# Performance work log

Measured on AMD Instinct MI355X. Metric: run time of the kernel, lower is better.

The kernel has to match this reference:

```python
import jax, jax.numpy as jnp
import numpy as np
from jax import lax

KH, KW = 3, 3  # hardcoded in the original extract_patches sizes=(1,3,3,1)


def setup_inputs() -> dict:
    key = jax.random.key(0)
    k1, k2, k3 = jax.random.split(key, 3)
    B, H, W, C = 32, 56, 56, 128
    num_och = 256
    x = jax.random.normal(k1, (B, H, W, C), dtype=jnp.float32)
    w = jax.random.normal(k2, (num_och, KH * KW * C), dtype=jnp.float32) * 0.05
    b = jax.random.normal(k3, (num_och,), dtype=jnp.float32) * 0.05
    return {"x": x, "w": w, "b": b}


def reference(x, w, b):
    # Original: extract_patches (SAME, stride 1, 3x3) -> tile num_och times ->
    # elementwise multiply with w -> reduce_sum over patch axis -> + bias.
    # This is exactly a 3x3 SAME conv: patch layout is (ky, kx, cin) row-major,
    # matching tf.image.extract_patches depth ordering.
    num_och = w.shape[0]
    cin = x.shape[-1]
    # (num_och, KH*KW*C) -> (KH, KW, C, num_och) for HWIO kernel layout
    kernel = w.reshape(num_och, KH, KW, cin).transpose(1, 2, 3, 0)
    out = lax.conv_general_dilated(
        x, kernel,
        window_strides=(1, 1),
        padding="SAME",
        dimension_numbers=("NHWC", "HWIO", "NHWC"),
    )
    return out + b
```

## Files before the change

kernel.cpp:

```cpp
#include <hip/hip_runtime.h>
#include <hip/hip_bf16.h>

#define HH   56
#define WW_  56
#define CIN  128
#define OCH  256
#define NPIX (32*56*56)
#define NX   (NPIX*CIN)
#define NW   (OCH*9*CIN)
#define XB_BYTES ((size_t)NX*2)
#define WB_BYTES ((size_t)NW*2)
#define ZP_OFF   (XB_BYTES + WB_BYTES)
#define WS_NEEDED (ZP_OFF + 256)

#define BM 128
#define BN 128
#define THREADS 256

typedef __attribute__((ext_vector_type(8))) short bf16x8;
typedef __attribute__((ext_vector_type(4))) float f32x4;
typedef __attribute__((address_space(1))) void v_g;
typedef __attribute__((address_space(3))) void v_l;

__device__ __forceinline__ unsigned short f2bf(float f) {
  union { float f; unsigned u; } v; v.f = f;
  unsigned r = v.u + 0x7FFF + ((v.u >> 16) & 1);
  return (unsigned short)(r >> 16);
}

__global__ __launch_bounds__(256) void convert_kern(
    const float* __restrict__ x, const float* __restrict__ w,
    char* __restrict__ ws)
{
  if (blockIdx.x == 0 && threadIdx.x < 64)
    ((float*)(ws + ZP_OFF))[threadIdx.x] = 0.f;

  unsigned short* out = (unsigned short*)ws;
  const int NT8 = (NX + NW) / 8;
  for (int i = blockIdx.x * blockDim.x + threadIdx.x; i < NT8;
       i += gridDim.x * blockDim.x) {
    const int e = i * 8;
    const float* src = (e < NX) ? (x + e) : (w + (e - NX));
    const float4 a = ((const float4*)src)[0];
    const float4 b = ((const float4*)src)[1];
    union { bf16x8 v; unsigned short u[8]; } p;
    p.u[0] = f2bf(a.x); p.u[1] = f2bf(a.y); p.u[2] = f2bf(a.z); p.u[3] = f2bf(a.w);
    p.u[4] = f2bf(b.x); p.u[5] = f2bf(b.y); p.u[6] = f2bf(b.z); p.u[7] = f2bf(b.w);
    *(bf16x8*)(out + e) = p.v;
  }
}

__global__ __launch_bounds__(THREADS, 2) void conv_gemm(
    const char* __restrict__ ws, const float* __restrict__ bias,
    float* __restrict__ out)
{
  __shared__ char lds[2][32768];

  const char* xb = ws;
  const char* wb = ws + XB_BYTES;
  const char* zp = ws + ZP_OFF;

  const int tid  = threadIdx.x;
  const int lane = tid & 63;
  const int wv   = tid >> 6;
  const int m0   = (blockIdx.x >> 1) * BM;
  const int n0   = (blockIdx.x & 1) * BN;

  int pixA[4]; int phA_[4]; int pwA_[4]; int chkA[4]; const char* bsrcB[4];
#pragma unroll
  for (int c = 0; c < 4; ++c) {
    const int rloc  = wv * 32 + c * 8 + (lane >> 3);
    const int chunk = ((lane & 7) ^ (rloc & 7)) * 16;
    chkA[c] = chunk;
    const int p   = m0 + rloc;
    const int pb  = p / (HH * WW_);
    const int phw = p - pb * (HH * WW_);
    phA_[c] = phw / WW_;
    pwA_[c] = phw - phA_[c] * WW_;
    pixA[c] = p;
    bsrcB[c] = wb + (size_t)(n0 + rloc) * (9 * CIN * 2) + chunk;
  }

  const int fr = lane & 15;
  const int fq = lane >> 4;
  const int wm = (wv >> 1) * 64;
  const int wn = (wv & 1) * 64;

  int aoff[2][4], boff[2][4];
#pragma unroll
  for (int ks = 0; ks < 2; ++ks)
#pragma unroll
    for (int i = 0; i < 4; ++i) {
      const int r = wm + i * 16 + fr;
      aoff[ks][i] = r * 128 + ((ks * 64 + fq * 16) ^ ((r & 7) << 4));
      const int c = wn + i * 16 + fr;
      boff[ks][i] = 16384 + c * 128 + ((ks * 64 + fq * 16) ^ ((c & 7) << 4));
    }

  f32x4 acc[4][4];
  const f32x4 zero4 = {0.f, 0.f, 0.f, 0.f};
#pragma unroll
  for (int i = 0; i < 4; ++i)
#pragma unroll
    for (int j = 0; j < 4; ++j) acc[i][j] = zero4;

#define STAGE(tt, bb) do {                                                   \
    const int kpos_ = (tt) >> 1, kc_ = (tt) & 1;                             \
    const int ky_ = kpos_ / 3;                                               \
    const int dy_ = ky_ - 1, dx_ = kpos_ - ky_ * 3 - 1;                      \
    _Pragma("unroll")                                                        \
    for (int c = 0; c < 4; ++c) {                                            \
      const int ih_ = phA_[c] + dy_, iw_ = pwA_[c] + dx_;                    \
      const bool v_ = ((unsigned)ih_ < (unsigned)HH) &                       \
                      ((unsigned)iw_ < (unsigned)WW_);                       \
      const char* ga_ = v_ ? (xb + (size_t)(pixA[c] + dy_ * WW_ + dx_) * 256 \
                                 + kc_ * 128 + chkA[c])                      \
                           : (zp + chkA[c]);                                 \
      __builtin_amdgcn_global_load_lds((const v_g*)ga_,                      \
          (v_l*)(&lds[bb][0] + wv * 4096 + c * 1024), 16, 0, 0);             \
      const char* gb_ = bsrcB[c] + (tt) * 128;                               \
      __builtin_amdgcn_global_load_lds((const v_g*)gb_,                      \
          (v_l*)(&lds[bb][16384] + wv * 4096 + c * 1024), 16, 0, 0);         \
    }                                                                        \
  } while (0)

  STAGE(0, 0);
  __syncthreads();

#pragma unroll 2
  for (int t = 0; t < 18; ++t) {
    if (t < 17) STAGE(t + 1, (t + 1) & 1);

    const char* base = &lds[t & 1][0];
    bf16x8 A[2][4], Bv[2][4];
#pragma unroll
    for (int ks = 0; ks < 2; ++ks)
#pragma unroll
      for (int i = 0; i < 4; ++i) {
        A[ks][i]  = *(const bf16x8*)(base + aoff[ks][i]);
        Bv[ks][i] = *(const bf16x8*)(base + boff[ks][i]);
      }
#pragma unroll
    for (int ks = 0; ks < 2; ++ks)
#pragma unroll
      for (int mi = 0; mi < 4; ++mi)
#pragma unroll
        for (int nj = 0; nj < 4; ++nj)
          acc[mi][nj] = __builtin_amdgcn_mfma_f32_16x16x32_bf16(
              A[ks][mi], Bv[ks][nj], acc[mi][nj], 0, 0, 0);

    __syncthreads();
  }
#undef STAGE

  float bv[4];
#pragma unroll
  for (int j = 0; j < 4; ++j) bv[j] = bias[n0 + wn + j * 16 + fr];

#pragma unroll
  for (int mi = 0; mi < 4; ++mi) {
#pragma unroll
    for (int j = 0; j < 4; ++j) {
      const int prow = m0 + wm + mi * 16 + fq * 4 + j;
      float* orow = out + (size_t)prow * OCH + n0 + wn + fr;
#pragma unroll
      for (int ni = 0; ni < 4; ++ni)
        orow[ni * 16] = acc[mi][ni][j] + bv[ni];
    }
  }
}

__global__ __launch_bounds__(THREADS) void conv3x3_mfma_fb(
    const float* __restrict__ x, const float* __restrict__ w,
    const float* __restrict__ bias, float* __restrict__ out)
{
  __shared__ alignas(16) unsigned char As[BM * 64];
  __shared__ alignas(16) unsigned char Bs[BN * 64];

  const int tid = threadIdx.x;
  const int m0 = (blockIdx.x >> 1) * BM;
  const int n0 = (blockIdx.x & 1) * BN;

  const int srow = tid >> 1;
  const int soff = (tid & 1) * 16;

  const int p   = m0 + srow;
  const int pb  = p / (HH * WW_);
  const int phw = p - pb * (HH * WW_);
  const int ph  = phw / WW_;
  const int pw  = phw - ph * WW_;

  const float* xrow = x + ((size_t)((pb * HH + ph) * WW_ + pw)) * CIN + soff;
  const float* wrow = w + (size_t)(n0 + srow) * (9 * CIN) + soff;

  const int sw0 = (srow * 64 + soff * 2)      ^ ((srow & 7) << 4);
  const int sw1 = (srow * 64 + soff * 2 + 16) ^ ((srow & 7) << 4);

  const int lane = tid & 63;
  const int wv = tid >> 6;
  const int wm = (wv >> 1) * 64;
  const int wn = (wv & 1) * 64;
  const int fr = lane & 15;
  const int fq = lane >> 4;

  int aoff[4], boff[4];
#pragma unroll
  for (int i = 0; i < 4; ++i) {
    const int r = wm + i * 16 + fr;
    aoff[i] = (r * 64 + fq * 16) ^ ((r & 7) << 4);
    const int c = wn + i * 16 + fr;
    boff[i] = (c * 64 + fq * 16) ^ ((c & 7) << 4);
  }

  f32x4 acc[4][4];
  const f32x4 zero4 = {0.f, 0.f, 0.f, 0.f};
#pragma unroll
  for (int i = 0; i < 4; ++i)
#pragma unroll
    for (int j = 0; j < 4; ++j) acc[i][j] = zero4;

#pragma unroll 1
  for (int kpos = 0; kpos < 9; ++kpos) {
    const int ky = kpos / 3;
    const int kx = kpos - ky * 3;
    const int ih = ph + ky - 1;
    const int iw = pw + kx - 1;
    const bool valid = ((unsigned)ih < (unsigned)HH) & ((unsigned)iw < (unsigned)WW_);
    const float* asrc = xrow + ((ky - 1) * WW_ + (kx - 1)) * CIN;
    const float* bsrc = wrow + kpos * CIN;

#pragma unroll 1
    for (int kc = 0; kc < 4; ++kc) {
      float4 a0, a1, a2, a3;
      if (valid) {
        const float4* s = (const float4*)(asrc + kc * 32);
        a0 = s[0]; a1 = s[1]; a2 = s[2]; a3 = s[3];
      } else {
        a0 = make_float4(0.f, 0.f, 0.f, 0.f);
        a1 = a0; a2 = a0; a3 = a0;
      }
      const float4* tql = (const float4*)(bsrc + kc * 32);
      const float4 b0 = tql[0], b1 = tql[1], b2 = tql[2], b3 = tql[3];

      __syncthreads();

      union { bf16x8 v; unsigned short u[8]; } pA0, pA1, pB0, pB1;
      pA0.u[0] = f2bf(a0.x); pA0.u[1] = f2bf(a0.y); pA0.u[2] = f2bf(a0.z); pA0.u[3] = f2bf(a0.w);
      pA0.u[4] = f2bf(a1.x); pA0.u[5] = f2bf(a1.y); pA0.u[6] = f2bf(a1.z); pA0.u[7] = f2bf(a1.w);
      pA1.u[0] = f2bf(a2.x); pA1.u[1] = f2bf(a2.y); pA1.u[2] = f2bf(a2.z); pA1.u[3] = f2bf(a2.w);
      pA1.u[4] = f2bf(a3.x); pA1.u[5] = f2bf(a3.y); pA1.u[6] = f2bf(a3.z); pA1.u[7] = f2bf(a3.w);
      pB0.u[0] = f2bf(b0.x); pB0.u[1] = f2bf(b0.y); pB0.u[2] = f2bf(b0.z); pB0.u[3] = f2bf(b0.w);
      pB0.u[4] = f2bf(b1.x); pB0.u[5] = f2bf(b1.y); pB0.u[6] = f2bf(b1.z); pB0.u[7] = f2bf(b1.w);
      pB1.u[0] = f2bf(b2.x); pB1.u[1] = f2bf(b2.y); pB1.u[2] = f2bf(b2.z); pB1.u[3] = f2bf(b2.w);
      pB1.u[4] = f2bf(b3.x); pB1.u[5] = f2bf(b3.y); pB1.u[6] = f2bf(b3.z); pB1.u[7] = f2bf(b3.w);

      *(bf16x8*)(As + sw0) = pA0.v;
      *(bf16x8*)(As + sw1) = pA1.v;
      *(bf16x8*)(Bs + sw0) = pB0.v;
      *(bf16x8*)(Bs + sw1) = pB1.v;

      __syncthreads();

      bf16x8 af[4], bfr[4];
#pragma unroll
      for (int i = 0; i < 4; ++i) af[i]  = *(const bf16x8*)(As + aoff[i]);
#pragma unroll
      for (int j = 0; j < 4; ++j) bfr[j] = *(const bf16x8*)(Bs + boff[j]);
#pragma unroll
      for (int i = 0; i < 4; ++i)
#pragma unroll
        for (int j = 0; j < 4; ++j)
          acc[i][j] = __builtin_amdgcn_mfma_f32_16x16x32_bf16(af[i], bfr[j], acc[i][j], 0, 0, 0);
    }
  }

  float bv[4];
#pragma unroll
  for (int j = 0; j < 4; ++j) bv[j] = bias[n0 + wn + j * 16 + fr];

#pragma unroll
  for (int mi = 0; mi < 4; ++mi) {
#pragma unroll
    for (int j = 0; j < 4; ++j) {
      const int prow = m0 + wm + mi * 16 + fq * 4 + j;
      float* orow = out + (size_t)prow * OCH + n0 + wn + fr;
#pragma unroll
      for (int ni = 0; ni < 4; ++ni)
        orow[ni * 16] = acc[mi][ni][j] + bv[ni];
    }
  }
}

extern "C" void kernel_launch(void* const* d_in, const int* in_sizes, int n_in,
                              void* d_out, int out_size, void* d_ws, size_t ws_size,
                              hipStream_t stream) {
  (void)in_sizes; (void)n_in; (void)out_size;
  const float* x = (const float*)d_in[0];
  const float* w = (const float*)d_in[1];
  const float* b = (const float*)d_in[2];
  float* out = (float*)d_out;

  if (ws_size >= WS_NEEDED) {
    convert_kern<<<dim3(2048), dim3(256), 0, stream>>>(x, w, (char*)d_ws);
    const int grid = (NPIX / BM) * (OCH / BN);
    conv_gemm<<<dim3(grid), dim3(THREADS), 0, stream>>>((const char*)d_ws, b, out);
  } else {
    const int grid = (NPIX / BM) * (OCH / BN);
    conv3x3_mfma_fb<<<dim3(grid), dim3(THREADS), 0, stream>>>(x, w, b, out);
  }
}
```

Baseline: 204.7 us.

## Triple-buffer conv GEMM with 512 threads and explicit waitcnt pipelining

Rewrites the implicit-GEMM conv kernel to use 8 waves per block (each computing a 64x32 sub-tile) and a three-slot LDS ring buffer. Loads are prefetched two stages ahead, and raw s_barrier plus partial vmcnt waits replace the full __syncthreads. MFMA sections run at raised wave priority. The aim is to hide global-to-LDS latency and raise occupancy per CU, at the cost of 96KB LDS per block and a fragile manual waitcnt schedule.

```diff
diff --git a/kernel.cpp b/kernel.cpp
--- a/kernel.cpp
+++ b/kernel.cpp
@@ -13,9 +13,9 @@
 #define ZP_OFF   (XB_BYTES + WB_BYTES)
 #define WS_NEEDED (ZP_OFF + 256)
 
-#define BM 128
-#define BN 128
-#define THREADS 256
+#define NT   18
+#define SLOT 32768
+#define THREADS 512
 
 typedef __attribute__((ext_vector_type(8))) short bf16x8;
 typedef __attribute__((ext_vector_type(4))) float f32x4;
@@ -50,11 +50,11 @@
   }
 }
 
-__global__ __launch_bounds__(THREADS, 2) void conv_gemm(
+__global__ __launch_bounds__(THREADS, 2) void conv_gemm3(
     const char* __restrict__ ws, const float* __restrict__ bias,
     float* __restrict__ out)
 {
-  __shared__ char lds[2][32768];
+  __shared__ char lds[3 * SLOT];
 
   const char* xb = ws;
   const char* wb = ws + XB_BYTES;
@@ -62,124 +62,158 @@
 
   const int tid  = threadIdx.x;
   const int lane = tid & 63;
-  const int wv   = tid >> 6;
-  const int m0   = (blockIdx.x >> 1) * BM;
-  const int n0   = (blockIdx.x & 1) * BN;
-
-  int pixA[4]; int phA_[4]; int pwA_[4]; int chkA[4]; const char* bsrcB[4];
-#pragma unroll
-  for (int c = 0; c < 4; ++c) {
-    const int rloc  = wv * 32 + c * 8 + (lane >> 3);
-    const int chunk = ((lane & 7) ^ (rloc & 7)) * 16;
-    chkA[c] = chunk;
-    const int p   = m0 + rloc;
-    const int pb  = p / (HH * WW_);
-    const int phw = p - pb * (HH * WW_);
-    phA_[c] = phw / WW_;
-    pwA_[c] = phw - phA_[c] * WW_;
-    pixA[c] = p;
-    bsrcB[c] = wb + (size_t)(n0 + rloc) * (9 * CIN * 2) + chunk;
+  const int m0   = (blockIdx.x >> 1) * 128;
+  const int n0   = (blockIdx.x & 1) * 128;
+
+  const int r0  = tid >> 3;
+  const int chk = ((tid & 7) ^ (r0 & 7)) * 16;
+  const char* zpc = zp + chk;
+
+  int pixA[2], phA[2], pwA[2];
+  const char* bsrc[2];
+#pragma unroll
+  for (int l = 0; l < 2; ++l) {
+    const int r  = r0 + l * 64;
+    const int p  = m0 + r;
+    const int pb = p / 3136;
+    const int phw = p - pb * 3136;
+    phA[l] = phw / 56;
+    pwA[l] = phw - phA[l] * 56;
+    pixA[l] = p;
+    bsrc[l] = wb + (size_t)(n0 + r) * 2304 + chk;
   }
 
   const int fr = lane & 15;
   const int fq = lane >> 4;
-  const int wm = (wv >> 1) * 64;
-  const int wn = (wv & 1) * 64;
-
-  int aoff[2][4], boff[2][4];
-#pragma unroll
-  for (int ks = 0; ks < 2; ++ks)
-#pragma unroll
-    for (int i = 0; i < 4; ++i) {
-      const int r = wm + i * 16 + fr;
-      aoff[ks][i] = r * 128 + ((ks * 64 + fq * 16) ^ ((r & 7) << 4));
-      const int c = wn + i * 16 + fr;
-      boff[ks][i] = 16384 + c * 128 + ((ks * 64 + fq * 16) ^ ((c & 7) << 4));
-    }
-
-  f32x4 acc[4][4];
+  const int wv = tid >> 6;
+  const int wr = wv >> 2;
+  const int wc = wv & 3;
+
+  int aoff[2][4], boff[2][2];
+#pragma unroll
+  for (int ks = 0; ks < 2; ++ks) {
+#pragma unroll
+    for (int mi = 0; mi < 4; ++mi) {
+      const int r = wr * 64 + mi * 16 + fr;
+      aoff[ks][mi] = r * 128 + ((ks * 64 + fq * 16) ^ ((r & 7) << 4));
+    }
+#pragma unroll
+    for (int nj = 0; nj < 2; ++nj) {
+      const int c = wc * 32 + nj * 16 + fr;
+      boff[ks][nj] = 16384 + c * 128 + ((ks * 64 + fq * 16) ^ ((c & 7) << 4));
+    }
+  }
+
+  f32x4 acc[4][2];
   const f32x4 zero4 = {0.f, 0.f, 0.f, 0.f};
 #pragma unroll
-  for (int i = 0; i < 4; ++i)
-#pragma unroll
-    for (int j = 0; j < 4; ++j) acc[i][j] = zero4;
-
-#define STAGE(tt, bb) do {                                                   \
-    const int kpos_ = (tt) >> 1, kc_ = (tt) & 1;                             \
-    const int ky_ = kpos_ / 3;                                               \
-    const int dy_ = ky_ - 1, dx_ = kpos_ - ky_ * 3 - 1;                      \
-    _Pragma("unroll")                                                        \
-    for (int c = 0; c < 4; ++c) {                                            \
-      const int ih_ = phA_[c] + dy_, iw_ = pwA_[c] + dx_;                    \
-      const bool v_ = ((unsigned)ih_ < (unsigned)HH) &                       \
-                      ((unsigned)iw_ < (unsigned)WW_);                       \
-      const char* ga_ = v_ ? (xb + (size_t)(pixA[c] + dy_ * WW_ + dx_) * 256 \
-                                 + kc_ * 128 + chkA[c])                      \
-                           : (zp + chkA[c]);                                 \
-      __builtin_amdgcn_global_load_lds((const v_g*)ga_,                      \
-          (v_l*)(&lds[bb][0] + wv * 4096 + c * 1024), 16, 0, 0);             \
-      const char* gb_ = bsrcB[c] + (tt) * 128;                               \
-      __builtin_amdgcn_global_load_lds((const v_g*)gb_,                      \
-          (v_l*)(&lds[bb][16384] + wv * 4096 + c * 1024), 16, 0, 0);         \
-    }                                                                        \
+  for (int mi = 0; mi < 4; ++mi)
+#pragma unroll
+    for (int nj = 0; nj < 2; ++nj) acc[mi][nj] = zero4;
+
+#define STAGE(tt, dst) do {                                                   \
+    const int kpos_ = (tt) >> 1, kh_ = (tt) & 1;                              \
+    const int ky_ = kpos_ / 3;                                                \
+    const int dy_ = ky_ - 1, dx_ = kpos_ - ky_ * 3 - 1;                       \
+    _Pragma("unroll")                                                         \
+    for (int l = 0; l < 2; ++l) {                                             \
+      const int ih_ = phA[l] + dy_, iw_ = pwA[l] + dx_;                       \
+      const bool v_ = ((unsigned)ih_ < 56u) & ((unsigned)iw_ < 56u);          \
+      const char* ga_ = v_ ? (xb + (size_t)(pixA[l] + dy_ * 56 + dx_) * 256   \
+                                 + kh_ * 128 + chk)                           \
+                           : zpc;                                             \
+      __builtin_amdgcn_global_load_lds((const v_g*)ga_,                       \
+          (v_l*)((dst) + l * 8192 + tid * 16), 16, 0, 0);                     \
+    }                                                                         \
+    _Pragma("unroll")                                                         \
+    for (int l = 0; l < 2; ++l)                                               \
+      __builtin_amdgcn_global_load_lds((const v_g*)(bsrc[l] + (tt) * 128),    \
+          (v_l*)((dst) + 16384 + l * 8192 + tid * 16), 16, 0, 0);             \
   } while (0)
 
-  STAGE(0, 0);
-  __syncthreads();
-
-#pragma unroll 2
-  for (int t = 0; t < 18; ++t) {
-    if (t < 17) STAGE(t + 1, (t + 1) & 1);
-
-    const char* base = &lds[t & 1][0];
-    bf16x8 A[2][4], Bv[2][4];
-#pragma unroll
-    for (int ks = 0; ks < 2; ++ks)
-#pragma unroll
-      for (int i = 0; i < 4; ++i) {
-        A[ks][i]  = *(const bf16x8*)(base + aoff[ks][i]);
-        Bv[ks][i] = *(const bf16x8*)(base + boff[ks][i]);
-      }
-#pragma unroll
-    for (int ks = 0; ks < 2; ++ks)
-#pragma unroll
-      for (int mi = 0; mi < 4; ++mi)
-#pragma unroll
-        for (int nj = 0; nj < 4; ++nj)
-          acc[mi][nj] = __builtin_amdgcn_mfma_f32_16x16x32_bf16(
-              A[ks][mi], Bv[ks][nj], acc[mi][nj], 0, 0, 0);
-
-    __syncthreads();
-  }
+#define COMPUTE(src) do {                                                     \
+    bf16x8 Af[2][4], Bf[2][2];                                                \
+    _Pragma("unroll")                                                         \
+    for (int ks = 0; ks < 2; ++ks) {                                          \
+      _Pragma("unroll")                                                       \
+      for (int mi = 0; mi < 4; ++mi)                                          \
+        Af[ks][mi] = *(const bf16x8*)((src) + aoff[ks][mi]);                  \
+      _Pragma("unroll")                                                       \
+      for (int nj = 0; nj < 2; ++nj)                                          \
+        Bf[ks][nj] = *(const bf16x8*)((src) + boff[ks][nj]);                  \
+    }                                                                         \
+    __builtin_amdgcn_s_setprio(1);                                            \
+    _Pragma("unroll")                                                         \
+    for (int ks = 0; ks < 2; ++ks)                                            \
+      _Pragma("unroll")                                                       \
+      for (int mi = 0; mi < 4; ++mi)                                          \
+        _Pragma("unroll")                                                     \
+        for (int nj = 0; nj < 2; ++nj)                                        \
+          acc[mi][nj] = __builtin_amdgcn_mfma_f32_16x16x32_bf16(              \
+              Af[ks][mi], Bf[ks][nj], acc[mi][nj], 0, 0, 0);                  \
+    __builtin_amdgcn_s_setprio(0);                                            \
+  } while (0)
+
+  char* p0 = lds;
+  char* p1 = lds + SLOT;
+  char* p2 = lds + 2 * SLOT;
+
+  STAGE(0, p0);
+  STAGE(1, p1);
+
+#pragma unroll
+  for (int t = 0; t < NT - 2; ++t) {
+    __builtin_amdgcn_s_barrier();
+    __builtin_amdgcn_sched_barrier(0);
+    STAGE(t + 2, p2);
+    asm volatile("s_waitcnt vmcnt(8)" ::: "memory");
+    __builtin_amdgcn_s_barrier();
+    __builtin_amdgcn_sched_barrier(0);
+    COMPUTE(p0);
+    char* tmp = p0; p0 = p1; p1 = p2; p2 = tmp;
+  }
+
+  asm volatile("s_waitcnt vmcnt(4)" ::: "memory");
+  __builtin_amdgcn_s_barrier();
+  __builtin_amdgcn_sched_barrier(0);
+  COMPUTE(p0);
+  { char* tmp = p0; p0 = p1; p1 = p2; p2 = tmp; }
+
+  asm volatile("s_waitcnt vmcnt(0)" ::: "memory");
+  __builtin_amdgcn_s_barrier();
+  __builtin_amdgcn_sched_barrier(0);
+  COMPUTE(p0);
+
 #undef STAGE
-
-  float bv[4];
-#pragma unroll
-  for (int j = 0; j < 4; ++j) bv[j] = bias[n0 + wn + j * 16 + fr];
+#undef COMPUTE
+
+  float bv[2];
+#pragma unroll
+  for (int nj = 0; nj < 2; ++nj) bv[nj] = bias[n0 + wc * 32 + nj * 16 + fr];
 
 #pragma unroll
   for (int mi = 0; mi < 4; ++mi) {
 #pragma unroll
     for (int j = 0; j < 4; ++j) {
-      const int prow = m0 + wm + mi * 16 + fq * 4 + j;
-      float* orow = out + (size_t)prow * OCH + n0 + wn + fr;
-#pragma unroll
-      for (int ni = 0; ni < 4; ++ni)
-        orow[ni * 16] = acc[mi][ni][j] + bv[ni];
-    }
-  }
-}
-
-__global__ __launch_bounds__(THREADS) void conv3x3_mfma_fb(
+      const int prow = m0 + wr * 64 + mi * 16 + fq * 4 + j;
+      float* orow = out + (size_t)prow * OCH + n0 + wc * 32 + fr;
+#pragma unroll
+      for (int nj = 0; nj < 2; ++nj)
+        orow[nj * 16] = acc[mi][nj][j] + bv[nj];
+    }
+  }
+}
+
+__global__ __launch_bounds__(256) void conv3x3_mfma_fb(
     const float* __restrict__ x, const float* __restrict__ w,
     const float* __restrict__ bias, float* __restrict__ out)
 {
-  __shared__ alignas(16) unsigned char As[BM * 64];
-  __shared__ alignas(16) unsigned char Bs[BN * 64];
+  __shared__ alignas(16) unsigned char As[128 * 64];
+  __shared__ alignas(16) unsigned char Bs[128 * 64];
 
   const int tid = threadIdx.x;
-  const int m0 = (blockIdx.x >> 1) * BM;
-  const int n0 = (blockIdx.x & 1) * BN;
+  const int m0 = (blockIdx.x >> 1) * 128;
+  const int n0 = (blockIdx.x & 1) * 128;
 
   const int srow = tid >> 1;
   const int soff = (tid & 1) * 16;
@@ -227,7 +261,7 @@
     const int iw = pw + kx - 1;
     const bool valid = ((unsigned)ih < (unsigned)HH) & ((unsigned)iw < (unsigned)WW_);
     const float* asrc = xrow + ((ky - 1) * WW_ + (kx - 1)) * CIN;
-    const float* bsrc = wrow + kpos * CIN;
+    const float* bsrc2 = wrow + kpos * CIN;
 
 #pragma unroll 1
     for (int kc = 0; kc < 4; ++kc) {
@@ -239,7 +273,7 @@
         a0 = make_float4(0.f, 0.f, 0.f, 0.f);
         a1 = a0; a2 = a0; a3 = a0;
       }
-      const float4* tql = (const float4*)(bsrc + kc * 32);
+      const float4* tql = (const float4*)(bsrc2 + kc * 32);
       const float4 b0 = tql[0], b1 = tql[1], b2 = tql[2], b3 = tql[3];
 
       __syncthreads();
@@ -300,12 +334,11 @@
   const float* b = (const float*)d_in[2];
   float* out = (float*)d_out;
 
+  const int grid = (NPIX / 128) * 2;
   if (ws_size >= WS_NEEDED) {
     convert_kern<<<dim3(2048), dim3(256), 0, stream>>>(x, w, (char*)d_ws);
-    const int grid = (NPIX / BM) * (OCH / BN);
-    conv_gemm<<<dim3(grid), dim3(THREADS), 0, stream>>>((const char*)d_ws, b, out);
+    conv_gemm3<<<dim3(grid), dim3(THREADS), 0, stream>>>((const char*)d_ws, b, out);
   } else {
-    const int grid = (NPIX / BM) * (OCH / BN);
-    conv3x3_mfma_fb<<<dim3(grid), dim3(THREADS), 0, stream>>>(x, w, b, out);
-  }
-}
+    conv3x3_mfma_fb<<<dim3(grid), dim3(256), 0, stream>>>(x, w, b, out);
+  }
+}
```

After: 211.6 us. +3.4%, slower.
